# Kernel optimization log

Hardware: AMD Instinct MI355X
Metric: run time of the kernel (lower is better)

## Reference

```python
import jax, jax.numpy as jnp
import numpy as np

QLEN, MLEN, BSZ, DM, NH, DH, DI = 512, 512, 8, 1024, 16, 64, 4096
KLEN = QLEN + MLEN
EPS = 1e-5
NEG = -1e30


def layer_norm(x, g, b):
    mu = jnp.mean(x, axis=-1, keepdims=True)
    var = jnp.mean(jnp.square(x - mu), axis=-1, keepdims=True)
    return (x - mu) * jax.lax.rsqrt(var + EPS) * g + b


def rel_shift(x):
    # x: [qlen, rlen, bsz, n_head] -> Transformer-XL relative shift
    q, r, b, n = x.shape
    zp = jnp.zeros((q, 1, b, n), x.dtype)
    xp = jnp.concatenate([zp, x], axis=1).reshape(r + 1, q, b, n)
    return xp[1:].reshape(q, r, b, n)


def setup_inputs() -> dict:
    key = jax.random.key(0)
    ks = jax.random.split(key, 12)
    inp = {
        "w": jax.random.normal(ks[0], (QLEN, BSZ, DM), jnp.float32),
        "r": jax.random.normal(ks[1], (KLEN, DM), jnp.float32),
        "mems": jax.random.normal(ks[2], (MLEN, BSZ, DM), jnp.float32),
        "w_qkv": jax.random.normal(ks[3], (DM, 3 * NH * DH), jnp.float32) * 0.02,
        "w_r": jax.random.normal(ks[4], (DM, NH * DH), jnp.float32) * 0.02,
        "w_o": jax.random.normal(ks[5], (NH * DH, DM), jnp.float32) * 0.02,
        "r_w_bias": jax.random.normal(ks[6], (NH, DH), jnp.float32) * 0.02,
        "r_r_bias": jax.random.normal(ks[7], (NH, DH), jnp.float32) * 0.02,
        "ln1_g": jnp.ones((DM,), jnp.float32),
        "ln1_b": jnp.zeros((DM,), jnp.float32),
        "ff_w1": jax.random.normal(ks[8], (DM, DI), jnp.float32) * 0.02,
        "ff_b1": jnp.zeros((DI,), jnp.float32),
        "ff_w2": jax.random.normal(ks[9], (DI, DM), jnp.float32) * 0.02,
        "ff_b2": jnp.zeros((DM,), jnp.float32),
        "ln2_g": jnp.ones((DM,), jnp.float32),
        "ln2_b": jnp.zeros((DM,), jnp.float32),
    }
    # causal mask with memory: query i (global pos MLEN+i) cannot attend to j > MLEN+i
    i = jnp.arange(QLEN)[:, None]
    j = jnp.arange(KLEN)[None, :]
    inp["attn_mask"] = j > (i + MLEN)
    return inp


def reference(w, r, mems, attn_mask, w_qkv, w_r, w_o, r_w_bias, r_r_bias,
              ln1_g, ln1_b, ff_w1, ff_b1, ff_w2, ff_b2, ln2_g, ln2_b):
    qlen, bsz = w.shape[0], w.shape[1]
    scale = 1.0 / (DH ** 0.5)
    cat = jnp.concatenate([mems, w], axis=0)                 # [klen, b, d]
    klen = cat.shape[0]
    heads = cat @ w_qkv                                      # [klen, b, 3*H*D]
    hq, hk, hv = jnp.split(heads, 3, axis=-1)
    hq = hq[-qlen:].reshape(qlen, bsz, NH, DH)
    hk = hk.reshape(klen, bsz, NH, DH)
    hv = hv.reshape(klen, bsz, NH, DH)
    r_head_k = (r @ w_r).reshape(klen, NH, DH)               # [rlen, H, D]

    AC = jnp.einsum('ibnd,jbnd->ijbn', hq + r_w_bias, hk)
    BD = rel_shift(jnp.einsum('ibnd,jnd->ijbn', hq + r_r_bias, r_head_k))
    score = (AC + BD) * scale                                # [q, k, b, h]
    score = jnp.where(attn_mask[:, :, None, None], NEG, score)
    prob = jax.nn.softmax(score, axis=1)
    vec = jnp.einsum('ijbn,jbnd->ibnd', prob, hv).reshape(qlen, bsz, NH * DH)
    attn_out = vec @ w_o
    h = layer_norm(w + attn_out, ln1_g, ln1_b)               # post-LN
    ff = jax.nn.relu(h @ ff_w1 + ff_b1) @ ff_w2 + ff_b2
    return layer_norm(h + ff, ln2_g, ln2_b)
```

## Files before the change

kernel.cpp:

```cpp
#include <hip/hip_runtime.h>
#include <hip/hip_bf16.h>

#define QLEN 512
#define MLEN 512
#define KLEN 1024
#define BSZ 8
#define DM 1024
#define NH 16
#define DH 64
#define DI 4096
#define NEGF (-1e30f)

typedef unsigned short u16;
typedef __attribute__((ext_vector_type(8))) short short8;
typedef __attribute__((ext_vector_type(4))) short s16x4;
typedef __attribute__((ext_vector_type(4))) float f32x4;

__device__ __forceinline__ float bf2f(u16 u) {
    union { unsigned i; float f; } x; x.i = ((unsigned)u) << 16; return x.f;
}
__device__ __forceinline__ u16 f2bf(float f) {
    __hip_bfloat16 h = __float2bfloat16(f);
    return *reinterpret_cast<u16*>(&h);
}
__device__ __forceinline__ float4 ldg4(const float* p) {
    return *reinterpret_cast<const float4*>(p);
}
__device__ __forceinline__ void gload16(const void* g, void* l) {
    __builtin_amdgcn_global_load_lds(
        (const __attribute__((address_space(1))) void*)g,
        (__attribute__((address_space(3))) void*)l, 16, 0, 0);
}

__global__ __launch_bounds__(256) void cast2_kernel(
    const float* __restrict__ a, const float* __restrict__ b, int splitE,
    u16* __restrict__ out, int n)
{
    int idx = (blockIdx.x * 256 + threadIdx.x) * 4;
    if (idx >= n) return;
    const float* src = (idx < splitE) ? (a + idx) : (b + (idx - splitE));
    float4 v = ldg4(src);
    u16 o[4] = { f2bf(v.x), f2bf(v.y), f2bf(v.z), f2bf(v.w) };
    *reinterpret_cast<uint2*>(&out[idx]) = *reinterpret_cast<uint2*>(o);
}

__device__ __forceinline__ void tr32(
    const float* __restrict__ W, u16* __restrict__ WT, int K, int N, int k0, int n0)
{
    __shared__ float tile[32][33];
    const int tx = threadIdx.x & 31, ty = threadIdx.x >> 5;
    #pragma unroll
    for (int j = 0; j < 4; ++j)
        tile[ty + j * 8][tx] = W[(size_t)(k0 + ty + j * 8) * N + n0 + tx];
    __syncthreads();
    #pragma unroll
    for (int j = 0; j < 4; ++j)
        WT[(size_t)(n0 + ty + j * 8) * K + k0 + tx] = f2bf(tile[tx][ty + j * 8]);
}

__global__ __launch_bounds__(256) void transpose_all(
    const float* __restrict__ w_qkv, u16* __restrict__ qkvT,
    const float* __restrict__ w_r,   u16* __restrict__ wrT,
    const float* __restrict__ w_o,   u16* __restrict__ woT,
    const float* __restrict__ ffw1,  u16* __restrict__ f1T,
    const float* __restrict__ ffw2,  u16* __restrict__ f2T)
{
    int id = blockIdx.x;
    if (id < 3072)       { int l = id;        tr32(w_qkv, qkvT, 1024, 3072, (l / 96) * 32, (l % 96) * 32); }
    else if (id < 4096)  { int l = id - 3072; tr32(w_r,   wrT,  1024, 1024, (l / 32) * 32, (l % 32) * 32); }
    else if (id < 5120)  { int l = id - 4096; tr32(w_o,   woT,  1024, 1024, (l / 32) * 32, (l % 32) * 32); }
    else if (id < 9216)  { int l = id - 5120; tr32(ffw1,  f1T,  1024, 4096, (l / 128) * 32, (l % 128) * 32); }
    else                 { int l = id - 9216; tr32(ffw2,  f2T,  4096, 1024, (l / 32) * 32, (l % 32) * 32); }
}

__global__ __launch_bounds__(256) void v_transpose(
    const u16* __restrict__ heads, u16* __restrict__ Vg)
{
    const int bn = blockIdx.x;
    const int b = bn >> 4, n = bn & 15;
    const int kt = blockIdx.y;
    const int t = threadIdx.x;
    __shared__ u16 L[64 * 64];

    #pragma unroll
    for (int rep = 0; rep < 2; ++rep) {
        int idx = t + rep * 256;
        int key = idx >> 3, dc = (idx & 7) * 8;
        short8 v = *reinterpret_cast<const short8*>(
            &heads[((size_t)((kt * 64 + key) * BSZ + b)) * 3072 + 2048 + n * 64 + dc]);
        *reinterpret_cast<short8*>((char*)L + key * 128 + ((dc * 2) ^ ((key & 7) << 4))) = v;
    }
    __syncthreads();
    #pragma unroll
    for (int rep = 0; rep < 2; ++rep) {
        int idx = t + rep * 256;
        int d = idx >> 3, kc = (idx & 7) * 8;
        short8 o;
        #pragma unroll
        for (int e = 0; e < 8; ++e)
            o[e] = *(const short*)((char*)L + (kc + e) * 128 + ((d * 2) ^ (((kc + e) & 7) << 4)));
        *reinterpret_cast<short8*>(&Vg[((size_t)(bn * 64 + d)) * KLEN + kt * 64 + kc]) = o;
    }
}

template<bool BIAS, bool RELU, bool OUTBF>
__global__ __launch_bounds__(256) void gemm_mfma(
    const u16* __restrict__ A, const u16* __restrict__ BT,
    const float* __restrict__ bias,
    float* __restrict__ Cf, u16* __restrict__ Cb,
    int M, int N, int K, int lda, int ldb)
{
    __shared__ u16 As[128 * 64];
    __shared__ u16 Bs[128 * 64];
    const int bm = blockIdx.y * 128, bn = blockIdx.x * 128;
    const int z = blockIdx.z;
    A  += (size_t)z * K;
    BT += (size_t)z * K;
    const size_t zoff = (size_t)z * M * N;
    const int t = threadIdx.x;
    const int w = t >> 6, l = t & 63, lg = l >> 4, lq = l & 15;
    const int wm = (w >> 1) * 64, wn = (w & 1) * 64;
    const int r8 = l >> 3, slot = l & 7;
    const int gcol = (slot * 16) ^ (r8 << 4);

    f32x4 acc[4][4];
    #pragma unroll
    for (int x = 0; x < 4; ++x)
        #pragma unroll
        for (int y = 0; y < 4; ++y)
            acc[x][y] = (f32x4){0.f, 0.f, 0.f, 0.f};

    const int swzr = (lq & 7) << 4;

    for (int k0 = 0; k0 < K; k0 += 64) {
        __syncthreads();
        #pragma unroll
        for (int it = 0; it < 4; ++it) {
            const int base_row = w * 8 + it * 32;
            gload16((const char*)A + (((size_t)(bm + base_row + r8) * lda + k0) << 1) + gcol,
                    (char*)As + base_row * 128);
            gload16((const char*)BT + (((size_t)(bn + base_row + r8) * ldb + k0) << 1) + gcol,
                    (char*)Bs + base_row * 128);
        }
        __syncthreads();
        #pragma unroll
        for (int ks = 0; ks < 2; ++ks) {
            const int cb = (ks * 64 + 16 * lg) ^ swzr;
            short8 af[4], bf_[4];
            #pragma unroll
            for (int x = 0; x < 4; ++x)
                af[x] = *reinterpret_cast<const short8*>((char*)As + (wm + 16 * x + lq) * 128 + cb);
            #pragma unroll
            for (int y = 0; y < 4; ++y)
                bf_[y] = *reinterpret_cast<const short8*>((char*)Bs + (wn + 16 * y + lq) * 128 + cb);
            #pragma unroll
            for (int x = 0; x < 4; ++x)
                #pragma unroll
                for (int y = 0; y < 4; ++y)
                    acc[x][y] = __builtin_amdgcn_mfma_f32_16x16x32_bf16(af[x], bf_[y], acc[x][y], 0, 0, 0);
        }
    }
    #pragma unroll
    for (int x = 0; x < 4; ++x) {
        #pragma unroll
        for (int y = 0; y < 4; ++y) {
            const int col = bn + wn + 16 * y + lq;
            #pragma unroll
            for (int r = 0; r < 4; ++r) {
                const int row = bm + wm + 16 * x + 4 * lg + r;
                float v = acc[x][y][r];
                if constexpr (BIAS) { if (z == 0) v += bias[col]; }
                if constexpr (RELU) v = fmaxf(v, 0.f);
                if constexpr (OUTBF) Cb[zoff + (size_t)row * N + col] = f2bf(v);
                else                 Cf[zoff + (size_t)row * N + col] = v;
            }
        }
    }
}

template<bool BIAS, bool RELU, bool OUTBF>
__global__ __launch_bounds__(512, 2) void gemm_deep(
    const u16* __restrict__ A, const u16* __restrict__ BT,
    const float* __restrict__ bias,
    float* __restrict__ Cf, u16* __restrict__ Cb,
    int M, int N, int K, int lda, int ldb)
{
    __shared__ u16 lds[3 * 24576];
    const int bm = blockIdx.y * 256, bn = blockIdx.x * 128;
    const int z = blockIdx.z;
    A  += (size_t)z * K;
    BT += (size_t)z * K;
    const size_t zoff = (size_t)z * M * N;
    const int t = threadIdx.x;
    const int w = t >> 6, l = t & 63, lg = l >> 4, lq = l & 15;
    const int wm = (w >> 1) * 64;
    const int wn = (w & 1) * 64;
    const int srow = t >> 3, slot = t & 7;
    const int gcol = (slot * 16) ^ ((srow & 7) << 4);
    const int swzr = (lq & 7) << 4;

    auto stage_tile = [&](int kt, int buf) {
        const int k0 = kt * 64;
        char* Ab = (char*)lds + buf * 49152 + w * 1024;
        char* Bb = (char*)lds + buf * 49152 + 32768 + w * 1024;
        #pragma unroll
        for (int i = 0; i < 4; ++i)
            gload16((const char*)A + (((size_t)(bm + i * 64 + srow) * lda + k0) << 1) + gcol,
                    Ab + i * 8192);
        #pragma unroll
        for (int i = 0; i < 2; ++i)
            gload16((const char*)BT + (((size_t)(bn + i * 64 + srow) * ldb + k0) << 1) + gcol,
                    Bb + i * 8192);
    };

    f32x4 acc[4][4];
    #pragma unroll
    for (int x = 0; x < 4; ++x)
        #pragma unroll
        for (int y = 0; y < 4; ++y)
            acc[x][y] = (f32x4){0.f, 0.f, 0.f, 0.f};

    const int NT = K >> 6;
    stage_tile(0, 0);
    stage_tile(1, 1);

    for (int kt = 0; kt < NT; ++kt) {
        if (kt < NT - 1) asm volatile("s_waitcnt vmcnt(6)" ::: "memory");
        else             asm volatile("s_waitcnt vmcnt(0)" ::: "memory");
        __builtin_amdgcn_s_barrier();
        __builtin_amdgcn_sched_barrier(0);
        if (kt + 2 < NT) stage_tile(kt + 2, (kt + 2) % 3);

        const char* Ab = (const char*)lds + (kt % 3) * 49152;
        const char* Bb = Ab + 32768;
        #pragma unroll
        for (int ks = 0; ks < 2; ++ks) {
            const int cb = (ks * 64 + 16 * lg) ^ swzr;
            short8 af[4], bf_[4];
            #pragma unroll
            for (int x = 0; x < 4; ++x)
                af[x] = *reinterpret_cast<const short8*>(Ab + (wm + 16 * x + lq) * 128 + cb);
            #pragma unroll
            for (int y = 0; y < 4; ++y)
                bf_[y] = *reinterpret_cast<const short8*>(Bb + (wn + 16 * y + lq) * 128 + cb);
            __builtin_amdgcn_s_setprio(1);
            #pragma unroll
            for (int x = 0; x < 4; ++x)
                #pragma unroll
                for (int y = 0; y < 4; ++y)
                    acc[x][y] = __builtin_amdgcn_mfma_f32_16x16x32_bf16(af[x], bf_[y], acc[x][y], 0, 0, 0);
            __builtin_amdgcn_s_setprio(0);
        }
    }

    #pragma unroll
    for (int x = 0; x < 4; ++x) {
        #pragma unroll
        for (int y = 0; y < 4; ++y) {
            const int col = bn + wn + 16 * y + lq;
            #pragma unroll
            for (int r = 0; r < 4; ++r) {
                const int row = bm + wm + 16 * x + 4 * lg + r;
                float v = acc[x][y][r];
                if constexpr (BIAS) { if (z == 0) v += bias[col]; }
                if constexpr (RELU) v = fmaxf(v, 0.f);
                if constexpr (OUTBF) Cb[zoff + (size_t)row * N + col] = f2bf(v);
                else                 Cf[zoff + (size_t)row * N + col] = v;
            }
        }
    }
}

__global__ __launch_bounds__(512, 4) void attn_mfma(
    const u16* __restrict__ heads,
    const u16* __restrict__ Vg,
    const u16* __restrict__ rhk,
    const float* __restrict__ rwb, const float* __restrict__ rrb,
    u16* __restrict__ vec)
{
    const int b = blockIdx.x >> 4;
    const int n = blockIdx.x & 15;
    const int i0 = (3 - blockIdx.y) * 128;
    const int t = threadIdx.x;
    const int w = t >> 6;
    const int l = t & 63;
    const int lg = l >> 4, lq = l & 15;
    const int r8 = l >> 3, sl = l & 7;

    __shared__ u16 Ks[64 * 64];
    __shared__ u16 Vt[64 * 64];
    __shared__ u16 Rs[192 * 64];
    __shared__ u16 SbO[8 * 16 * 84];
    __shared__ u16 Ps[8 * 16 * 64];

    u16* SbW = SbO + w * 16 * 84;
    u16* PsW = Ps + w * 16 * 64;
    const int swzr = (lq & 7) << 4;
    const int stg_swz = (sl * 16) ^ (r8 << 4);

    short8 qw[2], qr[2];
    {
        const int qrow = i0 + 16 * w + lq;
        const size_t gbase = ((size_t)((MLEN + qrow) * BSZ + b)) * 3072 + n * 64;
        #pragma unroll
        for (int ks = 0; ks < 2; ++ks) {
            short8 qv = *reinterpret_cast<const short8*>(&heads[gbase + ks * 32 + 8 * lg]);
            short8 xw, xr;
            #pragma unroll
            for (int e = 0; e < 8; ++e) {
                float f = bf2f((u16)qv[e]);
                int d = ks * 32 + 8 * lg + e;
                xw[e] = (short)f2bf(f + rwb[n * 64 + d]);
                xr[e] = (short)f2bf(f + rrb[n * 64 + d]);
            }
            qw[ks] = xw; qr[ks] = xr;
        }
    }

    float m_run = NEGF, l_run = 0.f;
    f32x4 acc[4];
    #pragma unroll
    for (int df = 0; df < 4; ++df) acc[df] = (f32x4){0.f, 0.f, 0.f, 0.f};

    const int s0 = 112 - 16 * w;
    const int ntiles = i0 / 64 + 10;

    for (int tile = 0; tile < ntiles; ++tile) {
        const int j0 = tile << 6;
        __syncthreads();
        gload16((const char*)heads
                    + (((size_t)((j0 + w * 8 + r8) * BSZ + b)) * 3072 + 1024 + n * 64) * 2
                    + stg_swz,
                (char*)Ks + w * 1024);
        gload16((const char*)Vg
                    + (((size_t)(blockIdx.x * 64 + w * 8 + r8)) * KLEN + j0) * 2
                    + stg_swz,
                (char*)Vt + w * 1024);
        const int obase = j0 - i0 + 384;
        #pragma unroll
        for (int pass = 0; pass < 3; ++pass) {
            int row = pass * 64 + w * 8 + r8;
            int o = obase + row;
            o = o > (KLEN - 1) ? (KLEN - 1) : o;
            gload16((const char*)rhk + ((size_t)o * 1024 + n * 64) * 2 + stg_swz,
                    (char*)Rs + pass * 8192 + w * 1024);
        }
        __syncthreads();

        __builtin_amdgcn_s_setprio(1);
        #pragma unroll
        for (int ff = 0; ff < 5; ++ff) {
            f32x4 d = (f32x4){0.f, 0.f, 0.f, 0.f};
            #pragma unroll
            for (int ks = 0; ks < 2; ++ks) {
                short8 a = *reinterpret_cast<const short8*>(
                    (char*)Rs + (s0 + 16 * ff + lq) * 128 + ((ks * 64 + 16 * lg) ^ swzr));
                d = __builtin_amdgcn_mfma_f32_16x16x32_bf16(a, qr[ks], d, 0, 0, 0);
            }
            s16x4 pk;
            #pragma unroll
            for (int r = 0; r < 4; ++r) pk[r] = (short)f2bf(d[r]);
            *reinterpret_cast<s16x4*>(&SbW[lq * 84 + 16 * ff + 4 * lg]) = pk;
        }
        f32x4 dac[4];
        #pragma unroll
        for (int f = 0; f < 4; ++f) {
            f32x4 d = (f32x4){0.f, 0.f, 0.f, 0.f};
            #pragma unroll
            for (int ks = 0; ks < 2; ++ks) {
                short8 a = *reinterpret_cast<const short8*>(
                    (char*)Ks + (16 * f + lq) * 128 + ((ks * 64 + 16 * lg) ^ swzr));
                d = __builtin_amdgcn_mfma_f32_16x16x32_bf16(a, qw[ks], d, 0, 0, 0);
            }
            dac[f] = d;
        }
        __builtin_amdgcn_s_setprio(0);

        const bool fullTile = (i0 + 16 * w + MLEN - j0) >= 63;
        float sv[4][4];
        float mx = NEGF;
        if (fullTile) {
            #pragma unroll
            for (int f = 0; f < 4; ++f)
                #pragma unroll
                for (int r = 0; r < 4; ++r) {
                    int k = 16 * f + 4 * lg + r;
                    float bd = bf2f(SbW[lq * 84 + k - lq + 15]);
                    float x = (dac[f][r] + bd) * 0.125f;
                    sv[f][r] = x;
                    mx = fmaxf(mx, x);
                }
        } else {
            const int bound = i0 + 16 * w + lq + MLEN - j0;
            #pragma unroll
            for (int f = 0; f < 4; ++f)
                #pragma unroll
                for (int r = 0; r < 4; ++r) {
                    int k = 16 * f + 4 * lg + r;
                    float bd = bf2f(SbW[lq * 84 + k - lq + 15]);
                    float x = (k <= bound) ? (dac[f][r] + bd) * 0.125f : NEGF;
                    sv[f][r] = x;
                    mx = fmaxf(mx, x);
                }
        }
        mx = fmaxf(mx, __shfl_xor(mx, 16));
        mx = fmaxf(mx, __shfl_xor(mx, 32));
        float m_new = fmaxf(m_run, mx);
        float alpha = __expf(m_run - m_new);
        float ps = 0.f;
        #pragma unroll
        for (int f = 0; f < 4; ++f) {
            s16x4 pk;
            #pragma unroll
            for (int r = 0; r < 4; ++r) {
                float p = __expf(sv[f][r] - m_new);
                ps += p;
                pk[r] = (short)f2bf(p);
            }
            *reinterpret_cast<s16x4*>(
                (char*)PsW + lq * 128 + (((4 * f + lg) ^ ((lq & 7) << 1)) << 3)) = pk;
        }
        ps += __shfl_xor(ps, 16);
        ps += __shfl_xor(ps, 32);
        l_run = l_run * alpha + ps;
        m_run = m_new;

        float alr[4];
        #pragma unroll
        for (int r = 0; r < 4; ++r) alr[r] = __shfl(alpha, 20 * lg + r);
        __builtin_amdgcn_s_setprio(1);
        #pragma unroll
        for (int df = 0; df < 4; ++df) {
            f32x4 a = acc[df];
            #pragma unroll
            for (int r = 0; r < 4; ++r) a[r] *= alr[r];
            #pragma unroll
            for (int ks = 0; ks < 2; ++ks) {
                short8 pa = *reinterpret_cast<const short8*>(
                    (char*)PsW + lq * 128 + ((ks * 64 + 16 * lg) ^ swzr));
                short8 vb = *reinterpret_cast<const short8*>(
                    (char*)Vt + (16 * df + lq) * 128 + ((ks * 64 + 16 * lg) ^ swzr));
                a = __builtin_amdgcn_mfma_f32_16x16x32_bf16(pa, vb, a, 0, 0, 0);
            }
            acc[df] = a;
        }
        __builtin_amdgcn_s_setprio(0);
    }

    float inv[4];
    #pragma unroll
    for (int r = 0; r < 4; ++r) inv[r] = 1.f / __shfl(l_run, 20 * lg + r);
    #pragma unroll
    for (int df = 0; df < 4; ++df) {
        #pragma unroll
        for (int r = 0; r < 4; ++r) {
            const int il = 16 * w + 4 * lg + r;
            float o = acc[df][r] * inv[r];
            vec[((size_t)((i0 + il) * BSZ + b)) * DM + n * 64 + 16 * df + lq] = f2bf(o);
        }
    }
}

template<int NRES, bool WB>
__global__ __launch_bounds__(256) void ln_res_kernel(
    const float* __restrict__ x, const float* __restrict__ res,
    const float* __restrict__ res2,
    const float* __restrict__ g, const float* __restrict__ bta,
    float* __restrict__ out, u16* __restrict__ outb)
{
    const int row = blockIdx.x;
    const int t = threadIdx.x;
    const int lane = t & 63, wv = t >> 6;
    __shared__ float red0[4], red1[4];

    float4 a = ldg4(&x[(size_t)row * DM + t * 4]);
    float4 b = ldg4(&res[(size_t)row * DM + t * 4]);
    float v0 = a.x + b.x, v1 = a.y + b.y, v2 = a.z + b.z, v3 = a.w + b.w;
    if constexpr (NRES == 2) {
        float4 c = ldg4(&res2[(size_t)row * DM + t * 4]);
        v0 += c.x; v1 += c.y; v2 += c.z; v3 += c.w;
    }
    float s = v0 + v1 + v2 + v3;
    #pragma unroll
    for (int o = 32; o; o >>= 1) s += __shfl_xor(s, o);
    if (lane == 0) red0[wv] = s;
    __syncthreads();
    float mu = (red0[0] + red0[1] + red0[2] + red0[3]) * (1.f / DM);
    float d0 = v0 - mu, d1 = v1 - mu, d2 = v2 - mu, d3 = v3 - mu;
    float q = d0*d0 + d1*d1 + d2*d2 + d3*d3;
    #pragma unroll
    for (int o = 32; o; o >>= 1) q += __shfl_xor(q, o);
    if (lane == 0) red1[wv] = q;
    __syncthreads();
    float var = (red1[0] + red1[1] + red1[2] + red1[3]) * (1.f / DM);
    float rs = rsqrtf(var + 1e-5f);
    float4 gv = ldg4(&g[t * 4]);
    float4 bv = ldg4(&bta[t * 4]);
    float o0 = d0 * rs * gv.x + bv.x;
    float o1 = d1 * rs * gv.y + bv.y;
    float o2 = d2 * rs * gv.z + bv.z;
    float o3 = d3 * rs * gv.w + bv.w;
    float4 o4 = make_float4(o0, o1, o2, o3);
    *reinterpret_cast<float4*>(&out[(size_t)row * DM + t * 4]) = o4;
    if constexpr (WB) {
        u16 ob[4] = { f2bf(o0), f2bf(o1), f2bf(o2), f2bf(o3) };
        *reinterpret_cast<uint2*>(&outb[(size_t)row * DM + t * 4]) = *reinterpret_cast<uint2*>(ob);
    }
}

extern "C" void kernel_launch(void* const* d_in, const int* in_sizes, int n_in,
                              void* d_out, int out_size, void* d_ws, size_t ws_size,
                              hipStream_t stream) {
    const float* w     = (const float*)d_in[0];
    const float* r     = (const float*)d_in[1];
    const float* mems  = (const float*)d_in[2];
    const float* w_qkv = (const float*)d_in[3];
    const float* w_r   = (const float*)d_in[4];
    const float* w_o   = (const float*)d_in[5];
    const float* rwb   = (const float*)d_in[6];
    const float* rrb   = (const float*)d_in[7];
    const float* ln1g  = (const float*)d_in[8];
    const float* ln1b  = (const float*)d_in[9];
    const float* ffw1  = (const float*)d_in[10];
    const float* ffb1  = (const float*)d_in[11];
    const float* ffw2  = (const float*)d_in[12];
    const float* ffb2  = (const float*)d_in[13];
    const float* ln2g  = (const float*)d_in[14];
    const float* ln2b  = (const float*)d_in[15];
    (void)in_sizes; (void)n_in; (void)out_size; (void)ws_size;

    char* p = (char*)d_ws;
    auto alloc = [&](size_t bytes) { char* q = p; p += (bytes + 255) & ~(size_t)255; return q; };
    u16* catB   = (u16*)alloc((size_t)8192 * 1024 * 2);
    u16* rB     = (u16*)alloc((size_t)1024 * 1024 * 2);
    u16* qkvT   = (u16*)alloc((size_t)3072 * 1024 * 2);
    u16* wrT    = (u16*)alloc((size_t)1024 * 1024 * 2);
    u16* woT    = (u16*)alloc((size_t)1024 * 1024 * 2);
    u16* f1T    = (u16*)alloc((size_t)4096 * 1024 * 2);
    u16* f2T    = (u16*)alloc((size_t)1024 * 4096 * 2);
    u16* heads  = (u16*)alloc((size_t)8192 * 3072 * 2);
    u16* rhk    = (u16*)alloc((size_t)1024 * 1024 * 2);
    u16* vec    = (u16*)alloc((size_t)4096 * 1024 * 2);
    u16* hB     = (u16*)alloc((size_t)4096 * 1024 * 2);
    u16* ff1    = (u16*)alloc((size_t)4096 * 4096 * 2);
    float* hF   = (float*)alloc((size_t)4096 * 1024 * 4);

    u16* Vg = catB;
    float* attn_out = (float*)ff1;
    float* ff2 = (float*)heads;
    float* outp = (float*)d_out;

    cast2_kernel<<<8192, 256, 0, stream>>>(mems, w, 4096 * 1024, catB, 8192 * 1024);
    cast2_kernel<<<1024, 256, 0, stream>>>(r, r, 1024 * 1024, rB, 1024 * 1024);
    transpose_all<<<13312, 256, 0, stream>>>(w_qkv, qkvT, w_r, wrT, w_o, woT,
                                             ffw1, f1T, ffw2, f2T);

    gemm_deep<false, false, true><<<dim3(24, 32), 512, 0, stream>>>(
        catB, qkvT, nullptr, nullptr, heads, 8192, 3072, 1024, 1024, 1024);
    v_transpose<<<dim3(128, 16), 256, 0, stream>>>(heads, Vg);
    gemm_mfma<false, false, true><<<dim3(8, 8), 256, 0, stream>>>(
        rB, wrT, nullptr, nullptr, rhk, 1024, 1024, 1024, 1024, 1024);
    attn_mfma<<<dim3(BSZ * NH, QLEN / 128), 512, 0, stream>>>(
        heads, Vg, rhk, rwb, rrb, vec);
    gemm_mfma<false, false, false><<<dim3(8, 32, 2), 256, 0, stream>>>(
        vec, woT, nullptr, attn_out, nullptr, 4096, 1024, 512, 1024, 1024);
    ln_res_kernel<2, true><<<4096, 256, 0, stream>>>(
        w, attn_out, attn_out + (size_t)4096 * 1024, ln1g, ln1b, hF, hB);
    gemm_deep<true, true, true><<<dim3(32, 16), 512, 0, stream>>>(
        hB, f1T, ffb1, nullptr, ff1, 4096, 4096, 1024, 1024, 1024);
    gemm_deep<true, false, false><<<dim3(8, 16, 2), 512, 0, stream>>>(
        ff1, f2T, ffb2, ff2, nullptr, 4096, 1024, 2048, 4096, 4096);
    ln_res_kernel<2, false><<<4096, 256, 0, stream>>>(
        hF, ff2, ff2 + (size_t)4096 * 1024, ln2g, ln2b, outp, nullptr);
}
```

Before: 328.4 us.

## Ring-buffer relative-position tiles, skip fully masked warps, defer softmax rescaling

The attention kernel now keeps the relative-position key rows in a 256-row LDS ring buffer, so each tile after the first loads only 64 new rows instead of 192. The BD staging buffer and the probability buffer are merged into one per-warp LDS region to cut shared-memory footprint. Warps whose query rows are fully masked for a tile now skip that tile's compute. The online-softmax rescale of the accumulator is skipped when the new max stays within 8 of the running max, which risks larger exp values but keeps them bounded. The early continue after the barrier is safe because the next iteration starts with a sync that every warp reaches.

```diff
diff --git a/kernel.cpp b/kernel.cpp
--- a/kernel.cpp
+++ b/kernel.cpp
@@ -289,12 +289,10 @@
 
     __shared__ u16 Ks[64 * 64];
     __shared__ u16 Vt[64 * 64];
-    __shared__ u16 Rs[192 * 64];
-    __shared__ u16 SbO[8 * 16 * 84];
-    __shared__ u16 Ps[8 * 16 * 64];
-
-    u16* SbW = SbO + w * 16 * 84;
-    u16* PsW = Ps + w * 16 * 64;
+    __shared__ u16 Rs[256 * 64];
+    __shared__ u16 SbPs[8 * 16 * 88];
+
+    u16* SbW = SbPs + w * 16 * 88;
     const int swzr = (lq & 7) << 4;
     const int stg_swz = (sl * 16) ^ (r8 << 4);
 
@@ -323,6 +321,7 @@
     for (int df = 0; df < 4; ++df) acc[df] = (f32x4){0.f, 0.f, 0.f, 0.f};
 
     const int s0 = 112 - 16 * w;
+    const int rbase = 384 - i0;
     const int ntiles = i0 / 64 + 10;
 
     for (int tile = 0; tile < ntiles; ++tile) {
@@ -336,31 +335,43 @@
                     + (((size_t)(blockIdx.x * 64 + w * 8 + r8)) * KLEN + j0) * 2
                     + stg_swz,
                 (char*)Vt + w * 1024);
-        const int obase = j0 - i0 + 384;
-        #pragma unroll
-        for (int pass = 0; pass < 3; ++pass) {
-            int row = pass * 64 + w * 8 + r8;
-            int o = obase + row;
+        if (tile == 0) {
+            #pragma unroll
+            for (int pass = 0; pass < 3; ++pass) {
+                int row = pass * 64 + w * 8 + r8;
+                int o = rbase + row;
+                o = o > (KLEN - 1) ? (KLEN - 1) : o;
+                gload16((const char*)rhk + ((size_t)o * 1024 + n * 64) * 2 + stg_swz,
+                        (char*)Rs + row * 128);
+            }
+        } else {
+            int row = 128 + w * 8 + r8;
+            int o = rbase + j0 + row;
             o = o > (KLEN - 1) ? (KLEN - 1) : o;
+            int slot = (j0 + row) & 255;
             gload16((const char*)rhk + ((size_t)o * 1024 + n * 64) * 2 + stg_swz,
-                    (char*)Rs + pass * 8192 + w * 1024);
+                    (char*)Rs + slot * 128);
         }
         __syncthreads();
 
+        const int bmax = i0 + 16 * w + 15 + MLEN - j0;
+        if (bmax < 0) continue;
+
         __builtin_amdgcn_s_setprio(1);
         #pragma unroll
         for (int ff = 0; ff < 5; ++ff) {
+            const int slot = (j0 + s0 + 16 * ff + lq) & 255;
             f32x4 d = (f32x4){0.f, 0.f, 0.f, 0.f};
             #pragma unroll
             for (int ks = 0; ks < 2; ++ks) {
                 short8 a = *reinterpret_cast<const short8*>(
-                    (char*)Rs + (s0 + 16 * ff + lq) * 128 + ((ks * 64 + 16 * lg) ^ swzr));
+                    (char*)Rs + slot * 128 + ((ks * 64 + 16 * lg) ^ swzr));
                 d = __builtin_amdgcn_mfma_f32_16x16x32_bf16(a, qr[ks], d, 0, 0, 0);
             }
             s16x4 pk;
             #pragma unroll
             for (int r = 0; r < 4; ++r) pk[r] = (short)f2bf(d[r]);
-            *reinterpret_cast<s16x4*>(&SbW[lq * 84 + 16 * ff + 4 * lg]) = pk;
+            *reinterpret_cast<s16x4*>(&SbW[lq * 88 + 16 * ff + 4 * lg]) = pk;
         }
         f32x4 dac[4];
         #pragma unroll
@@ -385,7 +396,7 @@
                 #pragma unroll
                 for (int r = 0; r < 4; ++r) {
                     int k = 16 * f + 4 * lg + r;
-                    float bd = bf2f(SbW[lq * 84 + k - lq + 15]);
+                    float bd = bf2f(SbW[lq * 88 + k - lq + 15]);
                     float x = (dac[f][r] + bd) * 0.125f;
                     sv[f][r] = x;
                     mx = fmaxf(mx, x);
@@ -397,7 +408,7 @@
                 #pragma unroll
                 for (int r = 0; r < 4; ++r) {
                     int k = 16 * f + 4 * lg + r;
-                    float bd = bf2f(SbW[lq * 84 + k - lq + 15]);
+                    float bd = bf2f(SbW[lq * 88 + k - lq + 15]);
                     float x = (k <= bound) ? (dac[f][r] + bd) * 0.125f : NEGF;
                     sv[f][r] = x;
                     mx = fmaxf(mx, x);
@@ -405,8 +416,8 @@
         }
         mx = fmaxf(mx, __shfl_xor(mx, 16));
         mx = fmaxf(mx, __shfl_xor(mx, 32));
-        float m_new = fmaxf(m_run, mx);
-        float alpha = __expf(m_run - m_new);
+        const bool defer = (__all(mx <= m_run + 8.0f) != 0);
+        const float m_new = defer ? m_run : fmaxf(m_run, mx);
         float ps = 0.f;
         #pragma unroll
         for (int f = 0; f < 4; ++f) {
@@ -418,26 +429,33 @@
                 pk[r] = (short)f2bf(p);
             }
             *reinterpret_cast<s16x4*>(
-                (char*)PsW + lq * 128 + (((4 * f + lg) ^ ((lq & 7) << 1)) << 3)) = pk;
+                (char*)SbW + lq * 176 + (((4 * f + lg) ^ ((lq & 7) << 1)) << 3)) = pk;
         }
         ps += __shfl_xor(ps, 16);
         ps += __shfl_xor(ps, 32);
-        l_run = l_run * alpha + ps;
-        m_run = m_new;
-
-        float alr[4];
-        #pragma unroll
-        for (int r = 0; r < 4; ++r) alr[r] = __shfl(alpha, 20 * lg + r);
+        if (defer) {
+            l_run += ps;
+        } else {
+            float alpha = __expf(m_run - m_new);
+            l_run = l_run * alpha + ps;
+            m_run = m_new;
+            float alr[4];
+            #pragma unroll
+            for (int r = 0; r < 4; ++r) alr[r] = __shfl(alpha, 20 * lg + r);
+            #pragma unroll
+            for (int df = 0; df < 4; ++df)
+                #pragma unroll
+                for (int r = 0; r < 4; ++r) acc[df][r] *= alr[r];
+        }
+
         __builtin_amdgcn_s_setprio(1);
         #pragma unroll
         for (int df = 0; df < 4; ++df) {
             f32x4 a = acc[df];
             #pragma unroll
-            for (int r = 0; r < 4; ++r) a[r] *= alr[r];
-            #pragma unroll
             for (int ks = 0; ks < 2; ++ks) {
                 short8 pa = *reinterpret_cast<const short8*>(
-                    (char*)PsW + lq * 128 + ((ks * 64 + 16 * lg) ^ swzr));
+                    (char*)SbW + lq * 176 + ((ks * 64 + 16 * lg) ^ swzr));
                 short8 vb = *reinterpret_cast<const short8*>(
                     (char*)Vt + (16 * df + lq) * 128 + ((ks * 64 + 16 * lg) ^ swzr));
                 a = __builtin_amdgcn_mfma_f32_16x16x32_bf16(pa, vb, a, 0, 0, 0);
```

Result: no change. 329.8 us (+0.4%).

## Store QKV and R projections head-major, rotate R tiles, defer softmax rescale

Applied to the files above, without the earlier changes.

The QKV and R-projection GEMM epilogues now write outputs in a head-major [part][b*h][k][d] layout, so attention K/Q/R loads and the V transpose read contiguous 128-byte rows. The attention kernel keeps a 3-slot rotating buffer of R tiles and loads only one new R tile per iteration instead of three. It also skips fully masked tiles and defers the online-softmax rescale while the max grows by no more than 8. The costs are scattered 2-byte epilogue stores, more index arithmetic, and possible fp32 overflow risk from the deferred-max bound.

```diff
diff --git a/kernel.cpp b/kernel.cpp
--- a/kernel.cpp
+++ b/kernel.cpp
@@ -10,6 +10,7 @@
 #define DH 64
 #define DI 4096
 #define NEGF (-1e30f)
+#define HM_PART ((size_t)8388608)
 
 typedef unsigned short u16;
 typedef __attribute__((ext_vector_type(8))) short short8;
@@ -74,10 +75,9 @@
 }
 
 __global__ __launch_bounds__(256) void v_transpose(
-    const u16* __restrict__ heads, u16* __restrict__ Vg)
+    const u16* __restrict__ Vhm, u16* __restrict__ Vg)
 {
     const int bn = blockIdx.x;
-    const int b = bn >> 4, n = bn & 15;
     const int kt = blockIdx.y;
     const int t = threadIdx.x;
     __shared__ u16 L[64 * 64];
@@ -87,7 +87,7 @@
         int idx = t + rep * 256;
         int key = idx >> 3, dc = (idx & 7) * 8;
         short8 v = *reinterpret_cast<const short8*>(
-            &heads[((size_t)((kt * 64 + key) * BSZ + b)) * 3072 + 2048 + n * 64 + dc]);
+            &Vhm[((size_t)bn * 1024 + kt * 64 + key) * 64 + dc]);
         *reinterpret_cast<short8*>((char*)L + key * 128 + ((dc * 2) ^ ((key & 7) << 4))) = v;
     }
     __syncthreads();
@@ -103,7 +103,7 @@
     }
 }
 
-template<bool BIAS, bool RELU, bool OUTBF>
+template<bool BIAS, bool RELU, int OUT>
 __global__ __launch_bounds__(256) void gemm_mfma(
     const u16* __restrict__ A, const u16* __restrict__ BT,
     const float* __restrict__ bias,
@@ -160,6 +160,7 @@
                     acc[x][y] = __builtin_amdgcn_mfma_f32_16x16x32_bf16(af[x], bf_[y], acc[x][y], 0, 0, 0);
         }
     }
+    const int nn = ((bn + wn) >> 6) & 15;
     #pragma unroll
     for (int x = 0; x < 4; ++x) {
         #pragma unroll
@@ -171,14 +172,16 @@
                 float v = acc[x][y][r];
                 if constexpr (BIAS) { if (z == 0) v += bias[col]; }
                 if constexpr (RELU) v = fmaxf(v, 0.f);
-                if constexpr (OUTBF) Cb[zoff + (size_t)row * N + col] = f2bf(v);
-                else                 Cf[zoff + (size_t)row * N + col] = v;
-            }
-        }
-    }
-}
-
-template<bool BIAS, bool RELU, bool OUTBF>
+                if constexpr (OUT == 0) Cf[zoff + (size_t)row * N + col] = v;
+                else if constexpr (OUT == 1) Cb[zoff + (size_t)row * N + col] = f2bf(v);
+                else
+                    Cb[((size_t)nn * 1024 + row) * 64 + 16 * y + lq] = f2bf(v);
+            }
+        }
+    }
+}
+
+template<bool BIAS, bool RELU, int OUT>
 __global__ __launch_bounds__(512, 2) void gemm_deep(
     const u16* __restrict__ A, const u16* __restrict__ BT,
     const float* __restrict__ bias,
@@ -253,6 +256,8 @@
         }
     }
 
+    const int part = (bn + wn) >> 10;
+    const int nn = ((bn + wn) >> 6) & 15;
     #pragma unroll
     for (int x = 0; x < 4; ++x) {
         #pragma unroll
@@ -264,22 +269,28 @@
                 float v = acc[x][y][r];
                 if constexpr (BIAS) { if (z == 0) v += bias[col]; }
                 if constexpr (RELU) v = fmaxf(v, 0.f);
-                if constexpr (OUTBF) Cb[zoff + (size_t)row * N + col] = f2bf(v);
-                else                 Cf[zoff + (size_t)row * N + col] = v;
+                if constexpr (OUT == 0) Cf[zoff + (size_t)row * N + col] = v;
+                else if constexpr (OUT == 1) Cb[zoff + (size_t)row * N + col] = f2bf(v);
+                else {
+                    Cb[(size_t)part * HM_PART
+                       + ((size_t)((row & 7) * 16 + nn) * 1024 + (row >> 3)) * 64
+                       + 16 * y + lq] = f2bf(v);
+                }
             }
         }
     }
 }
 
 __global__ __launch_bounds__(512, 4) void attn_mfma(
-    const u16* __restrict__ heads,
+    const u16* __restrict__ Hm,
     const u16* __restrict__ Vg,
-    const u16* __restrict__ rhk,
+    const u16* __restrict__ rhm,
     const float* __restrict__ rwb, const float* __restrict__ rrb,
     u16* __restrict__ vec)
 {
-    const int b = blockIdx.x >> 4;
-    const int n = blockIdx.x & 15;
+    const int bnidx = blockIdx.x;
+    const int b = bnidx >> 4;
+    const int n = bnidx & 15;
     const int i0 = (3 - blockIdx.y) * 128;
     const int t = threadIdx.x;
     const int w = t >> 6;
@@ -287,6 +298,9 @@
     const int lg = l >> 4, lq = l & 15;
     const int r8 = l >> 3, sl = l & 7;
 
+    const u16* Qh = Hm;
+    const u16* Kh = Hm + HM_PART;
+
     __shared__ u16 Ks[64 * 64];
     __shared__ u16 Vt[64 * 64];
     __shared__ u16 Rs[192 * 64];
@@ -300,11 +314,10 @@
 
     short8 qw[2], qr[2];
     {
-        const int qrow = i0 + 16 * w + lq;
-        const size_t gbase = ((size_t)((MLEN + qrow) * BSZ + b)) * 3072 + n * 64;
+        const size_t qbase = ((size_t)bnidx * 1024 + MLEN + i0 + 16 * w + lq) * 64;
         #pragma unroll
         for (int ks = 0; ks < 2; ++ks) {
-            short8 qv = *reinterpret_cast<const short8*>(&heads[gbase + ks * 32 + 8 * lg]);
+            short8 qv = *reinterpret_cast<const short8*>(&Qh[qbase + ks * 32 + 8 * lg]);
             short8 xw, xr;
             #pragma unroll
             for (int e = 0; e < 8; ++e) {
@@ -323,38 +336,47 @@
     for (int df = 0; df < 4; ++df) acc[df] = (f32x4){0.f, 0.f, 0.f, 0.f};
 
     const int s0 = 112 - 16 * w;
+    const int rbase = 384 - i0;
     const int ntiles = i0 / 64 + 10;
 
     for (int tile = 0; tile < ntiles; ++tile) {
         const int j0 = tile << 6;
         __syncthreads();
-        gload16((const char*)heads
-                    + (((size_t)((j0 + w * 8 + r8) * BSZ + b)) * 3072 + 1024 + n * 64) * 2
-                    + stg_swz,
+        gload16((const char*)Kh + (((size_t)bnidx * 1024 + j0 + w * 8 + r8) * 64 << 1) + stg_swz,
                 (char*)Ks + w * 1024);
-        gload16((const char*)Vg
-                    + (((size_t)(blockIdx.x * 64 + w * 8 + r8)) * KLEN + j0) * 2
-                    + stg_swz,
+        gload16((const char*)Vg + ((((size_t)bnidx * 64 + w * 8 + r8) * KLEN + j0) << 1) + stg_swz,
                 (char*)Vt + w * 1024);
-        const int obase = j0 - i0 + 384;
-        #pragma unroll
-        for (int pass = 0; pass < 3; ++pass) {
-            int row = pass * 64 + w * 8 + r8;
-            int o = obase + row;
+        if (tile == 0) {
+            #pragma unroll
+            for (int pass = 0; pass < 3; ++pass) {
+                int row = pass * 64 + w * 8 + r8;
+                int o = rbase + row;
+                o = o > (KLEN - 1) ? (KLEN - 1) : o;
+                gload16((const char*)rhm + (((size_t)n * 1024 + o) * 64 << 1) + stg_swz,
+                        (char*)Rs + pass * 8192 + w * 1024);
+            }
+        } else {
+            const int g = tile + 2;
+            int o = rbase + g * 64 + w * 8 + r8;
             o = o > (KLEN - 1) ? (KLEN - 1) : o;
-            gload16((const char*)rhk + ((size_t)o * 1024 + n * 64) * 2 + stg_swz,
-                    (char*)Rs + pass * 8192 + w * 1024);
+            gload16((const char*)rhm + (((size_t)n * 1024 + o) * 64 << 1) + stg_swz,
+                    (char*)Rs + (g % 3) * 8192 + w * 1024);
         }
         __syncthreads();
 
+        const int bmax = i0 + 16 * w + 15 + MLEN - j0;
+        if (bmax < 0) continue;
+
         __builtin_amdgcn_s_setprio(1);
         #pragma unroll
         for (int ff = 0; ff < 5; ++ff) {
+            const int olf = s0 + 16 * ff;
+            const int srowb = ((tile + (olf >> 6)) % 3) * 64 + (olf & 63);
             f32x4 d = (f32x4){0.f, 0.f, 0.f, 0.f};
             #pragma unroll
             for (int ks = 0; ks < 2; ++ks) {
                 short8 a = *reinterpret_cast<const short8*>(
-                    (char*)Rs + (s0 + 16 * ff + lq) * 128 + ((ks * 64 + 16 * lg) ^ swzr));
+                    (char*)Rs + (srowb + lq) * 128 + ((ks * 64 + 16 * lg) ^ swzr));
                 d = __builtin_amdgcn_mfma_f32_16x16x32_bf16(a, qr[ks], d, 0, 0, 0);
             }
             s16x4 pk;
@@ -405,8 +427,8 @@
         }
         mx = fmaxf(mx, __shfl_xor(mx, 16));
         mx = fmaxf(mx, __shfl_xor(mx, 32));
-        float m_new = fmaxf(m_run, mx);
-        float alpha = __expf(m_run - m_new);
+        const bool defer = (__all(mx <= m_run + 8.0f) != 0);
+        const float m_new = defer ? m_run : fmaxf(m_run, mx);
         float ps = 0.f;
         #pragma unroll
         for (int f = 0; f < 4; ++f) {
@@ -422,18 +444,25 @@
         }
         ps += __shfl_xor(ps, 16);
         ps += __shfl_xor(ps, 32);
-        l_run = l_run * alpha + ps;
-        m_run = m_new;
-
-        float alr[4];
-        #pragma unroll
-        for (int r = 0; r < 4; ++r) alr[r] = __shfl(alpha, 20 * lg + r);
+        if (defer) {
+            l_run += ps;
+        } else {
+            float alpha = __expf(m_run - m_new);
+            l_run = l_run * alpha + ps;
+            m_run = m_new;
+            float alr[4];
+            #pragma unroll
+            for (int r = 0; r < 4; ++r) alr[r] = __shfl(alpha, 20 * lg + r);
+            #pragma unroll
+            for (int df = 0; df < 4; ++df)
+                #pragma unroll
+                for (int r = 0; r < 4; ++r) acc[df][r] *= alr[r];
+        }
+
         __builtin_amdgcn_s_setprio(1);
         #pragma unroll
         for (int df = 0; df < 4; ++df) {
             f32x4 a = acc[df];
-            #pragma unroll
-            for (int r = 0; r < 4; ++r) a[r] *= alr[r];
             #pragma unroll
             for (int ks = 0; ks < 2; ++ks) {
                 short8 pa = *reinterpret_cast<const short8*>(
@@ -538,8 +567,8 @@
     u16* woT    = (u16*)alloc((size_t)1024 * 1024 * 2);
     u16* f1T    = (u16*)alloc((size_t)4096 * 1024 * 2);
     u16* f2T    = (u16*)alloc((size_t)1024 * 4096 * 2);
-    u16* heads  = (u16*)alloc((size_t)8192 * 3072 * 2);
-    u16* rhk    = (u16*)alloc((size_t)1024 * 1024 * 2);
+    u16* headsHm= (u16*)alloc((size_t)3 * HM_PART * 2);
+    u16* rhkHm  = (u16*)alloc((size_t)1024 * 1024 * 2);
     u16* vec    = (u16*)alloc((size_t)4096 * 1024 * 2);
     u16* hB     = (u16*)alloc((size_t)4096 * 1024 * 2);
     u16* ff1    = (u16*)alloc((size_t)4096 * 4096 * 2);
@@ -547,7 +576,7 @@
 
     u16* Vg = catB;
     float* attn_out = (float*)ff1;
-    float* ff2 = (float*)heads;
+    float* ff2 = (float*)headsHm;
     float* outp = (float*)d_out;
 
     cast2_kernel<<<8192, 256, 0, stream>>>(mems, w, 4096 * 1024, catB, 8192 * 1024);
@@ -555,20 +584,20 @@
     transpose_all<<<13312, 256, 0, stream>>>(w_qkv, qkvT, w_r, wrT, w_o, woT,
                                              ffw1, f1T, ffw2, f2T);
 
-    gemm_deep<false, false, true><<<dim3(24, 32), 512, 0, stream>>>(
-        catB, qkvT, nullptr, nullptr, heads, 8192, 3072, 1024, 1024, 1024);
-    v_transpose<<<dim3(128, 16), 256, 0, stream>>>(heads, Vg);
-    gemm_mfma<false, false, true><<<dim3(8, 8), 256, 0, stream>>>(
-        rB, wrT, nullptr, nullptr, rhk, 1024, 1024, 1024, 1024, 1024);
+    gemm_deep<false, false, 2><<<dim3(24, 32), 512, 0, stream>>>(
+        catB, qkvT, nullptr, nullptr, headsHm, 8192, 3072, 1024, 1024, 1024);
+    v_transpose<<<dim3(128, 16), 256, 0, stream>>>(headsHm + 2 * HM_PART, Vg);
+    gemm_mfma<false, false, 3><<<dim3(8, 8), 256, 0, stream>>>(
+        rB, wrT, nullptr, nullptr, rhkHm, 1024, 1024, 1024, 1024, 1024);
     attn_mfma<<<dim3(BSZ * NH, QLEN / 128), 512, 0, stream>>>(
-        heads, Vg, rhk, rwb, rrb, vec);
-    gemm_mfma<false, false, false><<<dim3(8, 32, 2), 256, 0, stream>>>(
+        headsHm, Vg, rhkHm, rwb, rrb, vec);
+    gemm_mfma<false, false, 0><<<dim3(8, 32, 2), 256, 0, stream>>>(
         vec, woT, nullptr, attn_out, nullptr, 4096, 1024, 512, 1024, 1024);
     ln_res_kernel<2, true><<<4096, 256, 0, stream>>>(
         w, attn_out, attn_out + (size_t)4096 * 1024, ln1g, ln1b, hF, hB);
-    gemm_deep<true, true, true><<<dim3(32, 16), 512, 0, stream>>>(
+    gemm_deep<true, true, 1><<<dim3(32, 16), 512, 0, stream>>>(
         hB, f1T, ffb1, nullptr, ff1, 4096, 4096, 1024, 1024, 1024);
-    gemm_deep<true, false, false><<<dim3(8, 16, 2), 512, 0, stream>>>(
+    gemm_deep<true, false, 0><<<dim3(8, 16, 2), 512, 0, stream>>>(
         ff1, f2T, ffb2, ff2, nullptr, 4096, 1024, 2048, 4096, 4096);
     ln_res_kernel<2, false><<<4096, 256, 0, stream>>>(
         hF, ff2, ff2 + (size_t)4096 * 1024, ln2g, ln2b, outp, nullptr);
```

Result: no change. 327.0 us (-0.4%).
